# Kernel tuning notes

Measured on AMD Instinct MI355X. Metric: run time of the kernel, lower is better.

Reference implementation:

```python
import jax, jax.numpy as jnp
import numpy as np

IMG = 640
STRIDES = (8, 16, 32)
A = 5            # anchors per level
NC = 80          # num classes
IOU_TH = 0.5
NEG_RATIO = 1.0


def make_priors():
    scales = [1.0, 1.5, 2.0, 2.5, 3.0]
    out = []
    for s in STRIDES:
        f = IMG // s
        ys, xs = np.meshgrid(np.arange(f), np.arange(f), indexing='ij')
        cx = ((xs + 0.5) / f).ravel()
        cy = ((ys + 0.5) / f).ravel()
        for sc in scales:  # anchor-major to match merge_features (A, h, w) order
            wh = min(sc * 4.0 * s / IMG, 1.0)
            out.append(np.stack([cx, cy, np.full_like(cx, wh), np.full_like(cx, wh)], 1))
    return np.concatenate(out, 0).astype(np.float32)  # [42000, 4] cxcywh


def merge_features(feats):
    outs = []
    for feat in feats:
        n, c, h, w = feat.shape
        f = feat.reshape(n, A, c // A, h, w).transpose(0, 1, 3, 4, 2)
        outs.append(f.reshape(n, A * h * w, c // A))
    return jnp.concatenate(outs, axis=1)  # [n, M, 85]


def box_iou_cxcywh(a, b):
    # a [T,4], b [M,4] (cx,cy,w,h) -> IoU [T,M]
    a1 = jnp.concatenate([a[:, :2] - a[:, 2:] / 2, a[:, :2] + a[:, 2:] / 2], -1)
    b1 = jnp.concatenate([b[:, :2] - b[:, 2:] / 2, b[:, :2] + b[:, 2:] / 2], -1)
    tl = jnp.maximum(a1[:, None, :2], b1[None, :, :2])
    br = jnp.minimum(a1[:, None, 2:], b1[None, :, 2:])
    wh = jnp.clip(br - tl, 0.0)
    inter = wh[..., 0] * wh[..., 1]
    area_a = a[:, 2] * a[:, 3]
    area_b = b[:, 2] * b[:, 3]
    return inter / (area_a[:, None] + area_b[None, :] - inter + 1e-9)


def build_targets(targets, priors, batch):
    ious = box_iou_cxcywh(targets[:, 2:6], priors)  # [Nt, M]
    Nt, M = ious.shape
    img_ids = targets[:, 0].astype(jnp.int32)

    def per_image(i):
        valid = img_ids == i  # [Nt]
        iv = jnp.where(valid[:, None], ious, -1.0)
        best_gt_overlap = iv.max(0)            # [M]
        best_gt_idx = iv.argmax(0)             # [M]
        best_prior_idx = iv.argmax(1)          # [Nt]
        # torch: index_fill_(1) then sequential best_gt_overlap[best_prior_idx[j]] = j
        local_j = (jnp.cumsum(valid.astype(jnp.int32)) - 1).astype(jnp.float32)
        scat_idx = jnp.where(valid, best_prior_idx, M)  # drop invalid rows
        best_gt_overlap = best_gt_overlap.at[scat_idx].set(local_j, mode='drop')
        bbox = targets[best_gt_idx, 2:6]
        clss = targets[best_gt_idx, 1] + 1.0
        clss = jnp.where(best_gt_overlap < IOU_TH, 0.0, clss)
        t_xy = (bbox[:, :2] - priors[:, :2]) / priors[:, 2:]
        t_wh = jnp.log(bbox[:, 2:] / priors[:, 2:])
        return t_xy, t_wh, clss

    return jax.vmap(per_image)(jnp.arange(batch))  # [B,M,2],[B,M,2],[B,M]


def _smooth_l1(x):
    ax = jnp.abs(x)
    return jnp.where(ax < 1.0, 0.5 * ax * ax, ax - 0.5)


def compute_loss(preds, priors, targets):
    n, m, _ = preds.shape
    t_xy, t_wh, t_cls = build_targets(targets, priors, n)
    pos = t_cls > 0
    posf = pos.astype(preds.dtype)
    num_pos = posf.sum()

    # lbox: smooth L1 on xy and wh over positives (mean over pos*2 elements each)
    den2 = jnp.maximum(num_pos * 2.0, 1.0)
    lbox = (_smooth_l1(preds[..., 0:2] - t_xy) * posf[..., None]).sum() / den2 \
         + (_smooth_l1(preds[..., 2:4] - t_wh) * posf[..., None]).sum() / den2

    # lcls: cross entropy over positives, labels = t_cls - 1
    labels = jnp.clip(t_cls.astype(jnp.int32) - 1, 0, NC - 1)
    logz = jax.nn.log_softmax(preds[..., 5:], axis=-1)
    ce = -jnp.take_along_axis(logz, labels[..., None], axis=-1)[..., 0]
    lcls = (ce * posf).sum() / jnp.maximum(num_pos, 1.0)

    # hard negative mining (no grad): double argsort rank trick
    obj = preds[..., 4]
    loss_c = jax.lax.stop_gradient(-jax.nn.log_sigmoid(obj))
    loss_c = jnp.where(pos, 0.0, loss_c)
    order = jnp.argsort(-loss_c, axis=-1)
    rank = jnp.argsort(order, axis=-1)
    num_neg = jnp.minimum(NEG_RATIO * num_pos, m - num_pos)
    neg = rank.astype(preds.dtype) < num_neg
    sel = (pos | neg).astype(preds.dtype)

    # lobj: BCE-with-logits over pos|neg
    z = posf
    bce = jnp.maximum(obj, 0.0) - obj * z + jnp.log1p(jnp.exp(-jnp.abs(obj)))
    lobj = (bce * sel).sum() / jnp.maximum(sel.sum(), 1.0)

    loss = lbox + lcls + lobj
    return jnp.stack([loss, lbox, lobj, lcls])


def setup_inputs() -> dict:
    key = jax.random.key(0)
    ks = jax.random.split(key, 6)
    feat0 = jax.random.normal(ks[0], (8, 425, 80, 80), jnp.float32)
    feat1 = jax.random.normal(ks[1], (8, 425, 40, 40), jnp.float32)
    feat2 = jax.random.normal(ks[2], (8, 425, 20, 20), jnp.float32)
    B, T = 8, 20
    img = jnp.repeat(jnp.arange(B, dtype=jnp.float32), T)
    cls = jax.random.randint(ks[3], (B * T,), 0, NC).astype(jnp.float32)
    cxcy = jax.random.uniform(ks[4], (B * T, 2), minval=0.2, maxval=0.8)
    wh = jax.random.uniform(ks[5], (B * T, 2), minval=0.05, maxval=0.3)
    targets = jnp.concatenate([img[:, None], cls[:, None], cxcy, wh], 1)
    priors = jnp.asarray(make_priors())
    return {"feat0": feat0, "feat1": feat1, "feat2": feat2,
            "targets": targets, "priors": priors}


def reference(feat0, feat1, feat2, targets, priors):
    preds = merge_features([feat0, feat1, feat2])  # [8, 42000, 85]
    return compute_loss(preds, priors, targets)    # [loss, lbox, lobj, lcls]
```

## Files before the change

kernel.cpp:

```cpp
#include <hip/hip_runtime.h>
#include <math.h>

#define MTOT 42000
#define NB 8
#define NCLS 80
#define CAP_LIST 4096
#define MAXT 256
#define NT_MAX 2048
#define GX_MAIN 165
#define NBLK_MAIN (GX_MAIN*NB)
#define NCH 32
#define CS 1313

#define O_OVR 0
#define O_GIX (O_OVR + NB*MTOT*4)
#define O_LSC (O_GIX + NB*MTOT*4)
#define O_BCE (O_LSC + NB*MTOT*4)
#define O_BPI (O_BCE + NB*MTOT*4)
#define O_LJ  (O_BPI + NT_MAX*4)
#define O_LST (O_LJ + NT_MAX*4)
#define O_BPP (O_LST + NB*MAXT*4)
#define O_PA  (O_BPP + NT_MAX*NCH*8)
#define O_PN  (O_PA + NBLK_MAIN*16)
#define O_P2  (O_PN + NBLK_MAIN*4)
#define O_BINL (O_P2 + NBLK_MAIN*8)
#define O_CNT (O_BINL + NB*CAP_LIST*2*4)
#define O_HA  (((O_CNT + NB*4 + 255)/256)*256)
#define O_HB  (O_HA + NB*256*4)
#define O_ACC (O_HB + NB*256*4)
#define O_ACCI (O_ACC + 64)
#define O_ZEND (O_ACCI + 256)
#define ZWORDS ((O_ZEND - O_HA)/4)
#define ZBLK ((ZWORDS + 255)/256)

__device__ __forceinline__ float iou_cxcywh(float acx,float acy,float aw,float ah,
                                            float bcx,float bcy,float bw,float bh){
  float ax0=acx-aw*0.5f, ay0=acy-ah*0.5f, ax1=acx+aw*0.5f, ay1=acy+ah*0.5f;
  float bx0=bcx-bw*0.5f, by0=bcy-bh*0.5f, bx1=bcx+bw*0.5f, by1=bcy+bh*0.5f;
  float tlx=fmaxf(ax0,bx0), tly=fmaxf(ay0,by0);
  float brx=fminf(ax1,bx1), bry=fminf(ay1,by1);
  float wx=fmaxf(brx-tlx,0.f), wy=fmaxf(bry-tly,0.f);
  float inter=wx*wy;
  return inter/(aw*ah+bw*bh-inter+1e-9f);
}

__device__ __forceinline__ float sl1(float x){
  float ax=fabsf(x); return ax<1.f ? 0.5f*ax*ax : ax-0.5f;
}

__device__ __forceinline__ void feat_base(const float* f0,const float* f1,const float* f2,
                                          int i,int m,const float** basep,int* hwp){
  const float* fp; int hw, loc;
  if(m<32000){ fp=f0; hw=6400; loc=m; }
  else if(m<40000){ fp=f1; hw=1600; loc=m-32000; }
  else { fp=f2; hw=400; loc=m-40000; }
  int a=loc/hw, p=loc-a*hw;
  *basep = fp + (size_t)(i*425 + a*85)*(size_t)hw + p;
  *hwp = hw;
}

__global__ void k_init(const float* __restrict__ tg, int nt, int* __restrict__ list,
                       int* __restrict__ cnt, int* __restrict__ lj,
                       unsigned* __restrict__ zbase){
  int bx=blockIdx.x, tid=threadIdx.x;
  if(bx<ZBLK){
    int w=bx*256+tid;
    if(w<ZWORDS) zbase[w]=0u;
    return;
  }
  if(bx==ZBLK && tid<NB){
    int c=0;
    for(int q=0;q<nt;q++) if((int)tg[q*6]==tid) c++;
    cnt[tid]=c;
  }
  int t=(bx-ZBLK)*256+tid;
  if(t>=nt) return;
  int img=(int)tg[t*6];
  int j=0;
  for(int q=0;q<t;q++) if((int)tg[q*6]==img) j++;
  lj[t]=j;
  if(img>=0 && img<NB && j<MAXT) list[img*MAXT+j]=t;
}

__global__ void k_match(const float* __restrict__ tg, const float* __restrict__ priors,
                        const int* __restrict__ list, const int* __restrict__ cnt,
                        float* __restrict__ ovr, int* __restrict__ gix){
  __shared__ float st[MAXT*6];
  __shared__ int   sidx[MAXT];
  int i = blockIdx.y;
  int n = min(cnt[i],MAXT);
  for(int j=threadIdx.x;j<n;j+=blockDim.x){
    int t=list[i*MAXT+j];
    sidx[j]=t;
    #pragma unroll
    for(int q=0;q<6;q++) st[j*6+q]=tg[t*6+q];
  }
  __syncthreads();
  int m = blockIdx.x*blockDim.x + threadIdx.x;
  if(m>=MTOT) return;
  float4 pr = ((const float4*)priors)[m];
  float maxv=-1.0f; int bi=0;
  for(int j=0;j<n;j++){
    float v=iou_cxcywh(st[j*6+2],st[j*6+3],st[j*6+4],st[j*6+5], pr.x,pr.y,pr.z,pr.w);
    if(v>maxv){ maxv=v; bi=sidx[j]; }
  }
  ovr[i*MTOT+m]=maxv; gix[i*MTOT+m]=bi;
}

__global__ void k_bpA(const float* __restrict__ tg, const float* __restrict__ priors,
                      int nt, unsigned long long* __restrict__ part){
  __shared__ unsigned long long s[256];
  int t=blockIdx.y; if(t>=nt) return;
  int c=blockIdx.x;
  float acx=tg[t*6+2],acy=tg[t*6+3],aw=tg[t*6+4],ah=tg[t*6+5];
  int m0=c*CS, m1=min(m0+CS,MTOT);
  float bv=-1.f; int bm=0;
  for(int m=m0+threadIdx.x;m<m1;m+=blockDim.x){
    float4 pr=((const float4*)priors)[m];
    float v=iou_cxcywh(acx,acy,aw,ah,pr.x,pr.y,pr.z,pr.w);
    if(v>bv){ bv=v; bm=m; }
  }
  unsigned long long p = (bv<0.f) ? 0ull
      : (((unsigned long long)__float_as_uint(bv))<<32) | (unsigned)(~bm);
  s[threadIdx.x]=p;
  __syncthreads();
  for(int o=128;o>0;o>>=1){
    if(threadIdx.x<o){ if(s[threadIdx.x+o]>s[threadIdx.x]) s[threadIdx.x]=s[threadIdx.x+o]; }
    __syncthreads();
  }
  if(threadIdx.x==0) part[(size_t)t*NCH+c]=s[0];
}

__global__ void k_bpB(const unsigned long long* __restrict__ part, int nt,
                      int* __restrict__ bpi){
  __shared__ unsigned long long s[64];
  int t=blockIdx.x; if(t>=nt) return;
  int l=threadIdx.x;
  s[l]=(l<NCH)? part[(size_t)t*NCH+l] : 0ull;
  __syncthreads();
  for(int o=32;o>0;o>>=1){
    if(l<o){ if(s[l+o]>s[l]) s[l]=s[l+o]; }
    __syncthreads();
  }
  if(l==0) bpi[t]=~((unsigned)(s[0]&0xFFFFFFFFull));
}

__global__ void k_scatter(const float* __restrict__ tg, int nt,
                          const int* __restrict__ bpi, const int* __restrict__ lj,
                          float* __restrict__ ovr){
  int t=blockIdx.x*blockDim.x+threadIdx.x;
  if(t>=nt) return;
  int img=(int)tg[t*6];
  if(img<0||img>=NB) return;
  int myp=bpi[t];
  for(int q=t+1;q<nt;q++)
    if((int)tg[q*6]==img && bpi[q]==myp) return;
  ovr[img*MTOT+myp]=(float)lj[t];
}

__global__ void k_main(const float* __restrict__ f0,const float* __restrict__ f1,const float* __restrict__ f2,
                       const float* __restrict__ tg,const float* __restrict__ priors,
                       const float* __restrict__ ovr,const int* __restrict__ gix,
                       float* __restrict__ lsc,float* __restrict__ bcearr,
                       unsigned* __restrict__ histA,
                       float4* __restrict__ partA,int* __restrict__ partN){
  __shared__ unsigned h[256];
  __shared__ float sxy[4],swh[4],sbp[4],sce[4];
  __shared__ int snp[4];
  int tid=threadIdx.x;
  h[tid]=0;
  __syncthreads();
  int i=blockIdx.y;
  int m=blockIdx.x*blockDim.x+tid;
  int lane=tid&63, wid=tid>>6;
  bool valid=(m<MTOT);

  float lxy=0.f,lwh=0.f,bcep=0.f; int npos=0; bool pos=false; int gi=0;
  if(valid){
    int gid=i*MTOT+m;
    const float* base; int hw;
    feat_base(f0,f1,f2,i,m,&base,&hw);
    float ov=ovr[gid]; gi=gix[gid];
    float tc=tg[gi*6+1]+1.0f;
    pos=(ov>=0.5f)&&(tc>0.f);
    float obj=base[(size_t)4*hw];
    float sp=log1pf(expf(-fabsf(obj)));
    float bce=fmaxf(obj,0.f)-(pos?obj:0.f)+sp;
    float lc=pos?0.f:(fmaxf(-obj,0.f)+sp);
    lsc[gid]=lc; bcearr[gid]=bce;
    atomicAdd(&h[__float_as_uint(lc)>>24],1u);
    if(pos){
      npos=1; bcep=bce;
      float4 pr=((const float4*)priors)[m];
      float bx=tg[gi*6+2],by=tg[gi*6+3],bw=tg[gi*6+4],bh=tg[gi*6+5];
      float tx=(bx-pr.x)/pr.z, ty=(by-pr.y)/pr.w;
      float tw=logf(bw/pr.z), th=logf(bh/pr.w);
      lxy=sl1(base[0]-tx)+sl1(base[(size_t)hw]-ty);
      lwh=sl1(base[(size_t)2*hw]-tw)+sl1(base[(size_t)3*hw]-th);
    }
  }

  float wce=0.f;
  unsigned long long mask=__ballot(valid&&pos);
  while(mask){
    int s=__ffsll(mask)-1;
    mask&=mask-1;
    int m_s=__shfl(m,s);
    int gi_s=__shfl(gi,s);
    const float* bs; int hws;
    feat_base(f0,f1,f2,i,m_s,&bs,&hws);
    int label=(int)(tg[gi_s*6+1]+1.0f)-1;
    label=min(NCLS-1,max(0,label));
    float v0=bs[(size_t)(5+lane)*hws];
    float v1=(lane<16)?bs[(size_t)(69+lane)*hws]:-3.0e38f;
    float mx=fmaxf(v0,v1);
    #pragma unroll
    for(int o=32;o>0;o>>=1) mx=fmaxf(mx,__shfl_xor(mx,o));
    float se=expf(v0-mx)+((lane<16)?expf(v1-mx):0.f);
    float xl=((lane==label)?v0:0.f)+((lane<16&&lane+64==label)?v1:0.f);
    #pragma unroll
    for(int o=32;o>0;o>>=1){ se+=__shfl_xor(se,o); xl+=__shfl_xor(xl,o); }
    wce+=logf(se)+mx-xl;
  }

  #pragma unroll
  for(int o=32;o>0;o>>=1){
    lxy+=__shfl_xor(lxy,o); lwh+=__shfl_xor(lwh,o);
    bcep+=__shfl_xor(bcep,o); npos+=__shfl_xor(npos,o);
  }
  if(lane==0){ sxy[wid]=lxy; swh[wid]=lwh; sbp[wid]=bcep; sce[wid]=wce; snp[wid]=npos; }
  __syncthreads();
  unsigned c=h[tid];
  if(c) atomicAdd(&histA[i*256+tid],c);
  if(tid==0){
    float4 pa;
    pa.x=sxy[0]+sxy[1]+sxy[2]+sxy[3];
    pa.y=swh[0]+swh[1]+swh[2]+swh[3];
    pa.z=sce[0]+sce[1]+sce[2]+sce[3];
    pa.w=sbp[0]+sbp[1]+sbp[2]+sbp[3];
    int bid=blockIdx.y*gridDim.x+blockIdx.x;
    partA[bid]=pa;
    partN[bid]=snp[0]+snp[1]+snp[2]+snp[3];
  }
}

__global__ void k_redscanA(const float4* __restrict__ partA,const int* __restrict__ partN,
                           const unsigned* __restrict__ histA,
                           float* __restrict__ accf,int* __restrict__ acci){
  __shared__ int an[256];
  __shared__ float a0[256],a1[256],a2[256],a3[256];
  __shared__ unsigned a[256];
  int t=threadIdx.x, i=blockIdx.x;
  bool lead=(i==0);
  int n=0; float x=0,y=0,z=0,w=0;
  for(int b=t;b<NBLK_MAIN;b+=256){
    n+=partN[b];
    if(lead){ float4 p=partA[b]; x+=p.x; y+=p.y; z+=p.z; w+=p.w; }
  }
  an[t]=n;
  if(lead){ a0[t]=x; a1[t]=y; a2[t]=z; a3[t]=w; }
  __syncthreads();
  for(int o=128;o>0;o>>=1){
    if(t<o){
      an[t]+=an[t+o];
      if(lead){ a0[t]+=a0[t+o]; a1[t]+=a1[t+o]; a2[t]+=a2[t+o]; a3[t]+=a3[t+o]; }
    }
    __syncthreads();
  }
  int np=an[0];
  if(lead && t==0){ accf[0]=a0[0]; accf[1]=a1[0]; accf[2]=a2[0]; accf[3]=a3[0]; acci[0]=np; }
  a[t]=histA[i*256+t];
  __syncthreads();
  if(t==0){
    int k=min(np, MTOT-np);
    if(k<=0){ acci[2+i]=0x7fffffff; acci[10+i]=0; return; }
    int run=0;
    for(int c=255;c>=0;c--){
      int cb=(int)a[c];
      if(run<k && run+cb>=k){ acci[2+i]=c; acci[10+i]=k-run; return; }
      run+=cb;
    }
    acci[2+i]=0; acci[10+i]=k-run;
  }
}

__global__ void k_histB(const float* __restrict__ lsc, const int* __restrict__ acci,
                        unsigned* __restrict__ histB){
  __shared__ unsigned h[256];
  h[threadIdx.x]=0;
  __syncthreads();
  int i=blockIdx.y;
  int ca=acci[2+i];
  int m=blockIdx.x*blockDim.x+threadIdx.x;
  if(m<MTOT && ca!=0x7fffffff){
    unsigned u=__float_as_uint(lsc[i*MTOT+m]);
    if((int)(u>>24)==ca) atomicAdd(&h[(u>>16)&0xFF],1u);
  }
  __syncthreads();
  unsigned c=h[threadIdx.x];
  if(c) atomicAdd(&histB[i*256+threadIdx.x],c);
}

__device__ __forceinline__ void fine_scan(const unsigned* hb,int ca,int kres,int* bs_out,int* r_out){
  if(ca==0x7fffffff){ *bs_out=0x7fffffff; *r_out=0; return; }
  int run=0, bs=-1, r=0;
  for(int f=255;f>=0;f--){
    int cb=(int)hb[f];
    if(run<kres && run+cb>=kres){ bs=(ca<<8)|f; r=kres-run; break; }
    run+=cb;
  }
  if(bs<0){ bs=(ca<<8); r=kres-run; }
  *bs_out=bs; *r_out=r;
}

__global__ void k_select(const float* __restrict__ lsc,const float* __restrict__ bcearr,
                         const unsigned* __restrict__ histB,
                         int* __restrict__ acci,float2* __restrict__ part2,
                         int* __restrict__ binlist){
  __shared__ unsigned hb[256];
  __shared__ int sbs;
  __shared__ float ss[4]; __shared__ float sc[4];
  int tid=threadIdx.x, lane=tid&63, wid=tid>>6;
  int i=blockIdx.y;
  int ca=acci[2+i], kres=acci[10+i];
  hb[tid]=(ca==0x7fffffff)?0u:histB[i*256+tid];
  __syncthreads();
  if(tid==0){ int bs,r; fine_scan(hb,ca,kres,&bs,&r); sbs=bs; }
  __syncthreads();
  int bs_=sbs;
  int m=blockIdx.x*blockDim.x+tid;
  float s=0.f, c=0.f;
  if(m<MTOT){
    int gid=i*MTOT+m;
    unsigned u=__float_as_uint(lsc[gid]);
    int bin=(int)(u>>16);
    if(bin>bs_){ s=bcearr[gid]; c=1.f; }
    else if(bin==bs_){
      int idx=atomicAdd(&acci[18+i],1);
      if(idx<CAP_LIST){
        binlist[((size_t)i*CAP_LIST+idx)*2  ]=(int)u;
        binlist[((size_t)i*CAP_LIST+idx)*2+1]=gid;
      }
    }
  }
  #pragma unroll
  for(int o=32;o>0;o>>=1){ s+=__shfl_xor(s,o); c+=__shfl_xor(c,o); }
  if(lane==0){ ss[wid]=s; sc[wid]=c; }
  __syncthreads();
  if(tid==0) part2[blockIdx.y*gridDim.x+blockIdx.x]=make_float2(ss[0]+ss[1]+ss[2]+ss[3], sc[0]+sc[1]+sc[2]+sc[3]);
}

__global__ void k_ties(const float* __restrict__ bcearr,int* __restrict__ acci,
                       float* __restrict__ accf,const int* __restrict__ binlist,
                       const unsigned* __restrict__ histB){
  __shared__ unsigned hb[256];
  __shared__ int sbs, sr;
  int i=blockIdx.x, tid=threadIdx.x;
  int ca=acci[2+i], kres=acci[10+i];
  hb[tid]=(ca==0x7fffffff)?0u:histB[i*256+tid];
  __syncthreads();
  if(tid==0){ int bs,r; fine_scan(hb,ca,kres,&bs,&r); sbs=bs; sr=r; }
  __syncthreads();
  if(sbs==0x7fffffff) return;
  int n=min(acci[18+i],CAP_LIST);
  int r=sr;
  for(int e=tid;e<n;e+=blockDim.x){
    unsigned ue=(unsigned)binlist[((size_t)i*CAP_LIST+e)*2];
    int ge=binlist[((size_t)i*CAP_LIST+e)*2+1];
    int rank=0;
    for(int q=0;q<n;q++){
      unsigned uq=(unsigned)binlist[((size_t)i*CAP_LIST+q)*2];
      int gq=binlist[((size_t)i*CAP_LIST+q)*2+1];
      rank += ((uq>ue) || (uq==ue && gq<ge)) ? 1 : 0;
    }
    if(rank<r){
      atomicAdd(&accf[5], bcearr[ge]);
      atomicAdd(&acci[1], 1);
    }
  }
}

__global__ void k_final(const float* __restrict__ accf,const int* __restrict__ acci,
                        const float2* __restrict__ part2,float* __restrict__ out){
  __shared__ float ssum[256]; __shared__ float scnt[256];
  int t=threadIdx.x;
  float s=0.f,c=0.f;
  for(int b=t;b<NBLK_MAIN;b+=256){ float2 p=part2[b]; s+=p.x; c+=p.y; }
  ssum[t]=s; scnt[t]=c;
  __syncthreads();
  for(int o=128;o>0;o>>=1){
    if(t<o){ ssum[t]+=ssum[t+o]; scnt[t]+=scnt[t+o]; }
    __syncthreads();
  }
  if(t==0){
    int np=acci[0];
    float npf=(float)np;
    float den2=fmaxf(2.f*npf,1.f);
    float lbox=accf[0]/den2 + accf[1]/den2;
    float lcls=accf[2]/fmaxf(npf,1.f);
    float negsum=ssum[0]+accf[5];
    float negcnt=scnt[0]+(float)acci[1];
    float selc=npf+negcnt;
    float lobj=(accf[3]+negsum)/fmaxf(selc,1.f);
    out[0]=lbox+lcls+lobj;
    out[1]=lbox;
    out[2]=lobj;
    out[3]=lcls;
  }
}

extern "C" void kernel_launch(void* const* d_in, const int* in_sizes, int n_in,
                              void* d_out, int out_size, void* d_ws, size_t ws_size,
                              hipStream_t stream) {
  const float* f0=(const float*)d_in[0];
  const float* f1=(const float*)d_in[1];
  const float* f2=(const float*)d_in[2];
  const float* tg=(const float*)d_in[3];
  const float* priors=(const float*)d_in[4];
  int nt = in_sizes[3]/6;
  if(nt>NT_MAX) nt=NT_MAX;

  char* ws=(char*)d_ws;
  float*    ovr    =(float*)   (ws+O_OVR);
  int*      gix    =(int*)     (ws+O_GIX);
  float*    lsc    =(float*)   (ws+O_LSC);
  float*    bcearr =(float*)   (ws+O_BCE);
  int*      bpi    =(int*)     (ws+O_BPI);
  int*      lj     =(int*)     (ws+O_LJ);
  int*      list   =(int*)     (ws+O_LST);
  unsigned long long* bpp=(unsigned long long*)(ws+O_BPP);
  float4*   partA  =(float4*)  (ws+O_PA);
  int*      partN  =(int*)     (ws+O_PN);
  float2*   part2  =(float2*)  (ws+O_P2);
  int*      binlist=(int*)     (ws+O_BINL);
  int*      cnt    =(int*)     (ws+O_CNT);
  unsigned* histA  =(unsigned*)(ws+O_HA);
  unsigned* histB  =(unsigned*)(ws+O_HB);
  float*    accf   =(float*)   (ws+O_ACC);
  int*      acci   =(int*)     (ws+O_ACCI);
  unsigned* zbase  =(unsigned*)(ws+O_HA);

  int ntb=(nt+255)/256;
  k_init<<<ZBLK+ntb,256,0,stream>>>(tg,nt,list,cnt,lj,zbase);
  dim3 gm(GX_MAIN, NB);
  k_match<<<gm,256,0,stream>>>(tg,priors,list,cnt,ovr,gix);
  dim3 gbp(NCH, nt);
  k_bpA<<<gbp,256,0,stream>>>(tg,priors,nt,bpp);
  k_bpB<<<nt,64,0,stream>>>(bpp,nt,bpi);
  k_scatter<<<ntb,256,0,stream>>>(tg,nt,bpi,lj,ovr);
  k_main<<<gm,256,0,stream>>>(f0,f1,f2,tg,priors,ovr,gix,lsc,bcearr,histA,partA,partN);
  k_redscanA<<<NB,256,0,stream>>>(partA,partN,histA,accf,acci);
  k_histB<<<gm,256,0,stream>>>(lsc,acci,histB);
  k_select<<<gm,256,0,stream>>>(lsc,bcearr,histB,acci,part2,binlist);
  k_ties<<<NB,256,0,stream>>>(bcearr,acci,accf,binlist,histB);
  k_final<<<1,256,0,stream>>>(accf,acci,part2,(float*)d_out);
}
```

Measured before the change: 151.5 us.

## Merge independent stages into heterogeneous launches and cut kernel count

Several independent stages now share one launch with a per-block role: prior matching, objectness gathering and per-target best-prior search go into one grid, and the negative histogram pass runs alongside the positive box/class loss. The best-prior reduction and scatter collapse into one single-block kernel, and the tie resolution merges with the final reduction. The aim is to cut launch overhead and serialization across about eleven small kernels. In exchange it adds an extra objectness buffer round trip and serializes tie work into one block.

Result: slower. 247.2 us (+63.2%).

```diff
diff --git a/kernel.cpp b/kernel.cpp
--- a/kernel.cpp
+++ b/kernel.cpp
@@ -14,22 +14,21 @@
 
 #define O_OVR 0
 #define O_GIX (O_OVR + NB*MTOT*4)
-#define O_LSC (O_GIX + NB*MTOT*4)
+#define O_OBJ (O_GIX + NB*MTOT*4)
+#define O_LSC (O_OBJ + NB*MTOT*4)
 #define O_BCE (O_LSC + NB*MTOT*4)
-#define O_BPI (O_BCE + NB*MTOT*4)
-#define O_LJ  (O_BPI + NT_MAX*4)
-#define O_LST (O_LJ + NT_MAX*4)
-#define O_BPP (O_LST + NB*MAXT*4)
+#define O_LST (O_BCE + NB*MTOT*4)
+#define O_LJ  (O_LST + NB*MAXT*4)
+#define O_CNT (O_LJ + NT_MAX*4)
+#define O_BPP (((O_CNT + 64 + 7)/8)*8)
 #define O_PA  (O_BPP + NT_MAX*NCH*8)
 #define O_PN  (O_PA + NBLK_MAIN*16)
 #define O_P2  (O_PN + NBLK_MAIN*4)
 #define O_BINL (O_P2 + NBLK_MAIN*8)
-#define O_CNT (O_BINL + NB*CAP_LIST*2*4)
-#define O_HA  (((O_CNT + NB*4 + 255)/256)*256)
+#define O_HA  (((O_BINL + NB*CAP_LIST*2*4 + 255)/256)*256)
 #define O_HB  (O_HA + NB*256*4)
-#define O_ACC (O_HB + NB*256*4)
-#define O_ACCI (O_ACC + 64)
-#define O_ZEND (O_ACCI + 256)
+#define O_ACCI (O_HB + NB*256*4)
+#define O_ZEND (O_ACCI + 128)
 #define ZWORDS ((O_ZEND - O_HA)/4)
 #define ZBLK ((ZWORDS + 255)/256)
 
@@ -59,6 +58,18 @@
   *hwp = hw;
 }
 
+__device__ __forceinline__ void fine_scan(const unsigned* hb,int ca,int kres,int* bs_out,int* r_out){
+  if(ca==0x7fffffff){ *bs_out=0x7fffffff; *r_out=0; return; }
+  int run=0, bs=-1, r=0;
+  for(int f=255;f>=0;f--){
+    int cb=(int)hb[f];
+    if(run<kres && run+cb>=kres){ bs=(ca<<8)|f; r=kres-run; break; }
+    run+=cb;
+  }
+  if(bs<0){ bs=(ca<<8); r=kres-run; }
+  *bs_out=bs; *r_out=r;
+}
+
 __global__ void k_init(const float* __restrict__ tg, int nt, int* __restrict__ list,
                        int* __restrict__ cnt, int* __restrict__ lj,
                        unsigned* __restrict__ zbase){
@@ -82,235 +93,233 @@
   if(img>=0 && img<NB && j<MAXT) list[img*MAXT+j]=t;
 }
 
-__global__ void k_match(const float* __restrict__ tg, const float* __restrict__ priors,
-                        const int* __restrict__ list, const int* __restrict__ cnt,
-                        float* __restrict__ ovr, int* __restrict__ gix){
+__global__ void k_big1(const float* __restrict__ f0,const float* __restrict__ f1,const float* __restrict__ f2,
+                       const float* __restrict__ tg,const float* __restrict__ priors,
+                       const int* __restrict__ list,const int* __restrict__ cnt,int nt,
+                       float* __restrict__ ovr,int* __restrict__ gix,
+                       float* __restrict__ objc,unsigned long long* __restrict__ bpp){
   __shared__ float st[MAXT*6];
-  __shared__ int   sidx[MAXT];
-  int i = blockIdx.y;
-  int n = min(cnt[i],MAXT);
-  for(int j=threadIdx.x;j<n;j+=blockDim.x){
-    int t=list[i*MAXT+j];
-    sidx[j]=t;
-    #pragma unroll
-    for(int q=0;q<6;q++) st[j*6+q]=tg[t*6+q];
-  }
-  __syncthreads();
-  int m = blockIdx.x*blockDim.x + threadIdx.x;
-  if(m>=MTOT) return;
-  float4 pr = ((const float4*)priors)[m];
-  float maxv=-1.0f; int bi=0;
-  for(int j=0;j<n;j++){
-    float v=iou_cxcywh(st[j*6+2],st[j*6+3],st[j*6+4],st[j*6+5], pr.x,pr.y,pr.z,pr.w);
-    if(v>maxv){ maxv=v; bi=sidx[j]; }
-  }
-  ovr[i*MTOT+m]=maxv; gix[i*MTOT+m]=bi;
-}
-
-__global__ void k_bpA(const float* __restrict__ tg, const float* __restrict__ priors,
-                      int nt, unsigned long long* __restrict__ part){
-  __shared__ unsigned long long s[256];
-  int t=blockIdx.y; if(t>=nt) return;
-  int c=blockIdx.x;
-  float acx=tg[t*6+2],acy=tg[t*6+3],aw=tg[t*6+4],ah=tg[t*6+5];
-  int m0=c*CS, m1=min(m0+CS,MTOT);
-  float bv=-1.f; int bm=0;
-  for(int m=m0+threadIdx.x;m<m1;m+=blockDim.x){
+  __shared__ int sidx[MAXT];
+  __shared__ unsigned long long su[256];
+  int b=blockIdx.x, tid=threadIdx.x;
+  if(b<NBLK_MAIN){
+    int i=b/GX_MAIN, cb=b-(b/GX_MAIN)*GX_MAIN;
+    int n=min(cnt[i],MAXT);
+    for(int j=tid;j<n;j+=256){
+      int t=list[i*MAXT+j];
+      sidx[j]=t;
+      #pragma unroll
+      for(int q=0;q<6;q++) st[j*6+q]=tg[t*6+q];
+    }
+    __syncthreads();
+    int m=cb*256+tid;
+    if(m>=MTOT) return;
     float4 pr=((const float4*)priors)[m];
-    float v=iou_cxcywh(acx,acy,aw,ah,pr.x,pr.y,pr.z,pr.w);
-    if(v>bv){ bv=v; bm=m; }
-  }
-  unsigned long long p = (bv<0.f) ? 0ull
-      : (((unsigned long long)__float_as_uint(bv))<<32) | (unsigned)(~bm);
-  s[threadIdx.x]=p;
-  __syncthreads();
-  for(int o=128;o>0;o>>=1){
-    if(threadIdx.x<o){ if(s[threadIdx.x+o]>s[threadIdx.x]) s[threadIdx.x]=s[threadIdx.x+o]; }
-    __syncthreads();
-  }
-  if(threadIdx.x==0) part[(size_t)t*NCH+c]=s[0];
-}
-
-__global__ void k_bpB(const unsigned long long* __restrict__ part, int nt,
-                      int* __restrict__ bpi){
-  __shared__ unsigned long long s[64];
-  int t=blockIdx.x; if(t>=nt) return;
-  int l=threadIdx.x;
-  s[l]=(l<NCH)? part[(size_t)t*NCH+l] : 0ull;
-  __syncthreads();
-  for(int o=32;o>0;o>>=1){
-    if(l<o){ if(s[l+o]>s[l]) s[l]=s[l+o]; }
-    __syncthreads();
-  }
-  if(l==0) bpi[t]=~((unsigned)(s[0]&0xFFFFFFFFull));
-}
-
-__global__ void k_scatter(const float* __restrict__ tg, int nt,
-                          const int* __restrict__ bpi, const int* __restrict__ lj,
-                          float* __restrict__ ovr){
-  int t=blockIdx.x*blockDim.x+threadIdx.x;
-  if(t>=nt) return;
-  int img=(int)tg[t*6];
-  if(img<0||img>=NB) return;
-  int myp=bpi[t];
-  for(int q=t+1;q<nt;q++)
-    if((int)tg[q*6]==img && bpi[q]==myp) return;
-  ovr[img*MTOT+myp]=(float)lj[t];
-}
-
-__global__ void k_main(const float* __restrict__ f0,const float* __restrict__ f1,const float* __restrict__ f2,
-                       const float* __restrict__ tg,const float* __restrict__ priors,
-                       const float* __restrict__ ovr,const int* __restrict__ gix,
-                       float* __restrict__ lsc,float* __restrict__ bcearr,
-                       unsigned* __restrict__ histA,
-                       float4* __restrict__ partA,int* __restrict__ partN){
-  __shared__ unsigned h[256];
-  __shared__ float sxy[4],swh[4],sbp[4],sce[4];
-  __shared__ int snp[4];
-  int tid=threadIdx.x;
-  h[tid]=0;
-  __syncthreads();
-  int i=blockIdx.y;
-  int m=blockIdx.x*blockDim.x+tid;
-  int lane=tid&63, wid=tid>>6;
-  bool valid=(m<MTOT);
-
-  float lxy=0.f,lwh=0.f,bcep=0.f; int npos=0; bool pos=false; int gi=0;
-  if(valid){
-    int gid=i*MTOT+m;
+    float maxv=-1.f; int bi=0;
+    for(int j=0;j<n;j++){
+      float v=iou_cxcywh(st[j*6+2],st[j*6+3],st[j*6+4],st[j*6+5],pr.x,pr.y,pr.z,pr.w);
+      if(v>maxv){ maxv=v; bi=sidx[j]; }
+    }
+    ovr[i*MTOT+m]=maxv; gix[i*MTOT+m]=bi;
+  } else if(b<2*NBLK_MAIN){
+    int idx=b-NBLK_MAIN;
+    int i=idx/GX_MAIN, cb=idx-(idx/GX_MAIN)*GX_MAIN;
+    int m=cb*256+tid;
+    if(m>=MTOT) return;
     const float* base; int hw;
     feat_base(f0,f1,f2,i,m,&base,&hw);
-    float ov=ovr[gid]; gi=gix[gid];
-    float tc=tg[gi*6+1]+1.0f;
-    pos=(ov>=0.5f)&&(tc>0.f);
-    float obj=base[(size_t)4*hw];
+    objc[i*MTOT+m]=base[(size_t)4*hw];
+  } else {
+    int idx=b-2*NBLK_MAIN;
+    int t=idx/NCH, c=idx-(idx/NCH)*NCH;
+    float acx=tg[t*6+2],acy=tg[t*6+3],aw=tg[t*6+4],ah=tg[t*6+5];
+    int m0=c*CS, m1=min(m0+CS,MTOT);
+    float bv=-1.f; int bm=0;
+    for(int m=m0+tid;m<m1;m+=256){
+      float4 pr=((const float4*)priors)[m];
+      float v=iou_cxcywh(acx,acy,aw,ah,pr.x,pr.y,pr.z,pr.w);
+      if(v>bv){ bv=v; bm=m; }
+    }
+    unsigned long long p=(bv<0.f)?0ull
+        :(((unsigned long long)__float_as_uint(bv))<<32)|(unsigned)(~bm);
+    su[tid]=p;
+    __syncthreads();
+    for(int o=128;o>0;o>>=1){
+      if(tid<o){ if(su[tid+o]>su[tid]) su[tid]=su[tid+o]; }
+      __syncthreads();
+    }
+    if(tid==0) bpp[(size_t)t*NCH+c]=su[0];
+  }
+}
+
+__global__ void k_bpsc(const float* __restrict__ tg,int nt,
+                       const unsigned long long* __restrict__ bpp,
+                       const int* __restrict__ lj,float* __restrict__ ovr){
+  __shared__ int tbp[NT_MAX];
+  __shared__ int timg[NT_MAX];
+  int tid=threadIdx.x;
+  for(int t=tid;t<nt;t+=256){
+    unsigned long long best=0ull;
+    const unsigned long long* pp=&bpp[(size_t)t*NCH];
+    for(int c=0;c<NCH;c++){ unsigned long long v=pp[c]; if(v>best) best=v; }
+    int bm=~((unsigned)(best&0xFFFFFFFFull));
+    tbp[t]=min(max(bm,0),MTOT-1);
+    timg[t]=(int)tg[t*6];
+  }
+  __syncthreads();
+  for(int t=tid;t<nt;t+=256){
+    int img=timg[t];
+    if(img<0||img>=NB) continue;
+    int myp=tbp[t];
+    bool last=true;
+    for(int q=t+1;q<nt;q++) if(timg[q]==img&&tbp[q]==myp){ last=false; break; }
+    if(last) ovr[img*MTOT+myp]=(float)lj[t];
+  }
+}
+
+__global__ void k_lc(const float* __restrict__ tg,const float* __restrict__ objc,
+                     const float* __restrict__ ovr,const int* __restrict__ gix,int nt,
+                     float* __restrict__ lsc,float* __restrict__ bcearr,
+                     unsigned* __restrict__ histA,int* __restrict__ partN){
+  __shared__ unsigned h[256];
+  __shared__ int snp[4];
+  int tid=threadIdx.x, lane=tid&63, wid=tid>>6;
+  h[tid]=0u;
+  __syncthreads();
+  int i=blockIdx.y;
+  int m=blockIdx.x*256+tid;
+  int npos=0;
+  if(m<MTOT){
+    int gid=i*MTOT+m;
+    float ov=ovr[gid];
+    int gi=min(max(gix[gid],0),nt-1);
+    float tc=tg[gi*6+1]+1.f;
+    bool pos=(ov>=0.5f)&&(tc>0.f);
+    float obj=objc[gid];
     float sp=log1pf(expf(-fabsf(obj)));
     float bce=fmaxf(obj,0.f)-(pos?obj:0.f)+sp;
     float lc=pos?0.f:(fmaxf(-obj,0.f)+sp);
     lsc[gid]=lc; bcearr[gid]=bce;
     atomicAdd(&h[__float_as_uint(lc)>>24],1u);
-    if(pos){
-      npos=1; bcep=bce;
-      float4 pr=((const float4*)priors)[m];
-      float bx=tg[gi*6+2],by=tg[gi*6+3],bw=tg[gi*6+4],bh=tg[gi*6+5];
-      float tx=(bx-pr.x)/pr.z, ty=(by-pr.y)/pr.w;
-      float tw=logf(bw/pr.z), th=logf(bh/pr.w);
-      lxy=sl1(base[0]-tx)+sl1(base[(size_t)hw]-ty);
-      lwh=sl1(base[(size_t)2*hw]-tw)+sl1(base[(size_t)3*hw]-th);
-    }
-  }
-
-  float wce=0.f;
-  unsigned long long mask=__ballot(valid&&pos);
-  while(mask){
-    int s=__ffsll(mask)-1;
-    mask&=mask-1;
-    int m_s=__shfl(m,s);
-    int gi_s=__shfl(gi,s);
-    const float* bs; int hws;
-    feat_base(f0,f1,f2,i,m_s,&bs,&hws);
-    int label=(int)(tg[gi_s*6+1]+1.0f)-1;
-    label=min(NCLS-1,max(0,label));
-    float v0=bs[(size_t)(5+lane)*hws];
-    float v1=(lane<16)?bs[(size_t)(69+lane)*hws]:-3.0e38f;
-    float mx=fmaxf(v0,v1);
+    npos=pos?1:0;
+  }
+  #pragma unroll
+  for(int o=32;o>0;o>>=1) npos+=__shfl_xor(npos,o);
+  if(lane==0) snp[wid]=npos;
+  __syncthreads();
+  unsigned hc=h[tid];
+  if(hc) atomicAdd(&histA[i*256+tid],hc);
+  if(tid==0) partN[blockIdx.y*GX_MAIN+blockIdx.x]=snp[0]+snp[1]+snp[2]+snp[3];
+}
+
+__global__ void k_redscanA(const int* __restrict__ partN,const unsigned* __restrict__ histA,
+                           int* __restrict__ acci){
+  __shared__ int an[256];
+  __shared__ unsigned h[256];
+  int t=threadIdx.x, b=blockIdx.x;
+  int n=0;
+  for(int e=t;e<NBLK_MAIN;e+=256) n+=partN[e];
+  an[t]=n;
+  __syncthreads();
+  for(int o=128;o>0;o>>=1){ if(t<o) an[t]+=an[t+o]; __syncthreads(); }
+  int np=an[0];
+  if(b==0&&t==0) acci[0]=np;
+  h[t]=histA[b*256+t];
+  __syncthreads();
+  if(t==0){
+    int kk=min(np,MTOT-np);
+    if(kk<=0){ acci[2+b]=0x7fffffff; acci[10+b]=0; }
+    else{
+      int run=0, ca=-1, kres=0;
+      for(int c2=255;c2>=0;c2--){
+        int cbn=(int)h[c2];
+        if(run<kk&&run+cbn>=kk){ ca=c2; kres=kk-run; break; }
+        run+=cbn;
+      }
+      if(ca<0){ ca=0; kres=kk-run; }
+      acci[2+b]=ca; acci[10+b]=kres;
+    }
+  }
+}
+
+__global__ void k_big2(const float* __restrict__ f0,const float* __restrict__ f1,const float* __restrict__ f2,
+                       const float* __restrict__ tg,const float* __restrict__ priors,
+                       const float* __restrict__ ovr,const int* __restrict__ gix,
+                       const float* __restrict__ lsc,const float* __restrict__ bcearr,
+                       const int* __restrict__ acci,int nt,
+                       unsigned* __restrict__ histB,float4* __restrict__ partA){
+  __shared__ unsigned h[256];
+  __shared__ float rA[4],rB[4],rC[4],rD[4];
+  int b=blockIdx.x, tid=threadIdx.x, lane=tid&63, wid=tid>>6;
+  if(b<NBLK_MAIN){
+    h[tid]=0u;
+    __syncthreads();
+    int i=b/GX_MAIN, cb=b-(b/GX_MAIN)*GX_MAIN;
+    int ca=acci[2+i];
+    int m=cb*256+tid;
+    if(m<MTOT && ca!=0x7fffffff){
+      unsigned u=__float_as_uint(lsc[i*MTOT+m]);
+      if((int)(u>>24)==ca) atomicAdd(&h[(u>>16)&0xFF],1u);
+    }
+    __syncthreads();
+    unsigned c=h[tid];
+    if(c) atomicAdd(&histB[i*256+tid],c);
+  } else {
+    int idx=b-NBLK_MAIN;
+    int i=idx/GX_MAIN, cb=idx-(idx/GX_MAIN)*GX_MAIN;
+    int m=cb*256+tid;
+    bool valid=(m<MTOT);
+    float lxy=0.f,lwh=0.f,bcep=0.f,wce=0.f;
+    bool pos=false; int gi=0;
+    if(valid){
+      int gid=i*MTOT+m;
+      float ov=ovr[gid];
+      gi=min(max(gix[gid],0),nt-1);
+      float tc=tg[gi*6+1]+1.f;
+      pos=(ov>=0.5f)&&(tc>0.f);
+      if(pos){
+        const float* base; int hw;
+        feat_base(f0,f1,f2,i,m,&base,&hw);
+        bcep=bcearr[gid];
+        float4 pr=((const float4*)priors)[m];
+        float bx=tg[gi*6+2],by=tg[gi*6+3],bw=tg[gi*6+4],bh=tg[gi*6+5];
+        float tx=(bx-pr.x)/pr.z, ty=(by-pr.y)/pr.w;
+        float tw=logf(bw/pr.z), th=logf(bh/pr.w);
+        lxy=sl1(base[0]-tx)+sl1(base[(size_t)hw]-ty);
+        lwh=sl1(base[(size_t)2*hw]-tw)+sl1(base[(size_t)3*hw]-th);
+      }
+    }
+    unsigned long long mask=__ballot(valid&&pos);
+    while(mask){
+      int s=__ffsll(mask)-1;
+      mask&=mask-1;
+      int m_s=__shfl(m,s);
+      int gi_s=__shfl(gi,s);
+      const float* bs2; int hws;
+      feat_base(f0,f1,f2,i,m_s,&bs2,&hws);
+      int label=(int)(tg[gi_s*6+1]+1.f)-1;
+      label=min(NCLS-1,max(0,label));
+      float v0=bs2[(size_t)(5+lane)*hws];
+      float v1=(lane<16)?bs2[(size_t)(69+lane)*hws]:-3.0e38f;
+      float mx=fmaxf(v0,v1);
+      #pragma unroll
+      for(int o=32;o>0;o>>=1) mx=fmaxf(mx,__shfl_xor(mx,o));
+      float se=expf(v0-mx)+((lane<16)?expf(v1-mx):0.f);
+      float xl=((lane==label)?v0:0.f)+((lane<16&&lane+64==label)?v1:0.f);
+      #pragma unroll
+      for(int o=32;o>0;o>>=1){ se+=__shfl_xor(se,o); xl+=__shfl_xor(xl,o); }
+      wce+=logf(se)+mx-xl;
+    }
     #pragma unroll
-    for(int o=32;o>0;o>>=1) mx=fmaxf(mx,__shfl_xor(mx,o));
-    float se=expf(v0-mx)+((lane<16)?expf(v1-mx):0.f);
-    float xl=((lane==label)?v0:0.f)+((lane<16&&lane+64==label)?v1:0.f);
-    #pragma unroll
-    for(int o=32;o>0;o>>=1){ se+=__shfl_xor(se,o); xl+=__shfl_xor(xl,o); }
-    wce+=logf(se)+mx-xl;
-  }
-
-  #pragma unroll
-  for(int o=32;o>0;o>>=1){
-    lxy+=__shfl_xor(lxy,o); lwh+=__shfl_xor(lwh,o);
-    bcep+=__shfl_xor(bcep,o); npos+=__shfl_xor(npos,o);
-  }
-  if(lane==0){ sxy[wid]=lxy; swh[wid]=lwh; sbp[wid]=bcep; sce[wid]=wce; snp[wid]=npos; }
-  __syncthreads();
-  unsigned c=h[tid];
-  if(c) atomicAdd(&histA[i*256+tid],c);
-  if(tid==0){
-    float4 pa;
-    pa.x=sxy[0]+sxy[1]+sxy[2]+sxy[3];
-    pa.y=swh[0]+swh[1]+swh[2]+swh[3];
-    pa.z=sce[0]+sce[1]+sce[2]+sce[3];
-    pa.w=sbp[0]+sbp[1]+sbp[2]+sbp[3];
-    int bid=blockIdx.y*gridDim.x+blockIdx.x;
-    partA[bid]=pa;
-    partN[bid]=snp[0]+snp[1]+snp[2]+snp[3];
-  }
-}
-
-__global__ void k_redscanA(const float4* __restrict__ partA,const int* __restrict__ partN,
-                           const unsigned* __restrict__ histA,
-                           float* __restrict__ accf,int* __restrict__ acci){
-  __shared__ int an[256];
-  __shared__ float a0[256],a1[256],a2[256],a3[256];
-  __shared__ unsigned a[256];
-  int t=threadIdx.x, i=blockIdx.x;
-  bool lead=(i==0);
-  int n=0; float x=0,y=0,z=0,w=0;
-  for(int b=t;b<NBLK_MAIN;b+=256){
-    n+=partN[b];
-    if(lead){ float4 p=partA[b]; x+=p.x; y+=p.y; z+=p.z; w+=p.w; }
-  }
-  an[t]=n;
-  if(lead){ a0[t]=x; a1[t]=y; a2[t]=z; a3[t]=w; }
-  __syncthreads();
-  for(int o=128;o>0;o>>=1){
-    if(t<o){
-      an[t]+=an[t+o];
-      if(lead){ a0[t]+=a0[t+o]; a1[t]+=a1[t+o]; a2[t]+=a2[t+o]; a3[t]+=a3[t+o]; }
-    }
-    __syncthreads();
-  }
-  int np=an[0];
-  if(lead && t==0){ accf[0]=a0[0]; accf[1]=a1[0]; accf[2]=a2[0]; accf[3]=a3[0]; acci[0]=np; }
-  a[t]=histA[i*256+t];
-  __syncthreads();
-  if(t==0){
-    int k=min(np, MTOT-np);
-    if(k<=0){ acci[2+i]=0x7fffffff; acci[10+i]=0; return; }
-    int run=0;
-    for(int c=255;c>=0;c--){
-      int cb=(int)a[c];
-      if(run<k && run+cb>=k){ acci[2+i]=c; acci[10+i]=k-run; return; }
-      run+=cb;
-    }
-    acci[2+i]=0; acci[10+i]=k-run;
-  }
-}
-
-__global__ void k_histB(const float* __restrict__ lsc, const int* __restrict__ acci,
-                        unsigned* __restrict__ histB){
-  __shared__ unsigned h[256];
-  h[threadIdx.x]=0;
-  __syncthreads();
-  int i=blockIdx.y;
-  int ca=acci[2+i];
-  int m=blockIdx.x*blockDim.x+threadIdx.x;
-  if(m<MTOT && ca!=0x7fffffff){
-    unsigned u=__float_as_uint(lsc[i*MTOT+m]);
-    if((int)(u>>24)==ca) atomicAdd(&h[(u>>16)&0xFF],1u);
-  }
-  __syncthreads();
-  unsigned c=h[threadIdx.x];
-  if(c) atomicAdd(&histB[i*256+threadIdx.x],c);
-}
-
-__device__ __forceinline__ void fine_scan(const unsigned* hb,int ca,int kres,int* bs_out,int* r_out){
-  if(ca==0x7fffffff){ *bs_out=0x7fffffff; *r_out=0; return; }
-  int run=0, bs=-1, r=0;
-  for(int f=255;f>=0;f--){
-    int cb=(int)hb[f];
-    if(run<kres && run+cb>=kres){ bs=(ca<<8)|f; r=kres-run; break; }
-    run+=cb;
-  }
-  if(bs<0){ bs=(ca<<8); r=kres-run; }
-  *bs_out=bs; *r_out=r;
+    for(int o=32;o>0;o>>=1){
+      lxy+=__shfl_xor(lxy,o); lwh+=__shfl_xor(lwh,o); bcep+=__shfl_xor(bcep,o);
+    }
+    if(lane==0){ rA[wid]=lxy; rB[wid]=lwh; rC[wid]=wce; rD[wid]=bcep; }
+    __syncthreads();
+    if(tid==0)
+      partA[idx]=make_float4(rA[0]+rA[1]+rA[2]+rA[3], rB[0]+rB[1]+rB[2]+rB[3],
+                             rC[0]+rC[1]+rC[2]+rC[3], rD[0]+rD[1]+rD[2]+rD[3]);
+  }
 }
 
 __global__ void k_select(const float* __restrict__ lsc,const float* __restrict__ bcearr,
@@ -328,7 +337,7 @@
   if(tid==0){ int bs,r; fine_scan(hb,ca,kres,&bs,&r); sbs=bs; }
   __syncthreads();
   int bs_=sbs;
-  int m=blockIdx.x*blockDim.x+tid;
+  int m=blockIdx.x*256+tid;
   float s=0.f, c=0.f;
   if(m<MTOT){
     int gid=i*MTOT+m;
@@ -350,58 +359,69 @@
   if(tid==0) part2[blockIdx.y*gridDim.x+blockIdx.x]=make_float2(ss[0]+ss[1]+ss[2]+ss[3], sc[0]+sc[1]+sc[2]+sc[3]);
 }
 
-__global__ void k_ties(const float* __restrict__ bcearr,int* __restrict__ acci,
-                       float* __restrict__ accf,const int* __restrict__ binlist,
-                       const unsigned* __restrict__ histB){
+__global__ void k_tf(const float4* __restrict__ partA,const float2* __restrict__ part2,
+                     const float* __restrict__ bcearr,const unsigned* __restrict__ histB,
+                     const int* __restrict__ acci,const int* __restrict__ binlist,
+                     float* __restrict__ out){
+  __shared__ float a0[256],a1[256],a2[256],a3[256],s0[256],s1[256];
   __shared__ unsigned hb[256];
   __shared__ int sbs, sr;
-  int i=blockIdx.x, tid=threadIdx.x;
-  int ca=acci[2+i], kres=acci[10+i];
-  hb[tid]=(ca==0x7fffffff)?0u:histB[i*256+tid];
-  __syncthreads();
-  if(tid==0){ int bs,r; fine_scan(hb,ca,kres,&bs,&r); sbs=bs; sr=r; }
-  __syncthreads();
-  if(sbs==0x7fffffff) return;
-  int n=min(acci[18+i],CAP_LIST);
-  int r=sr;
-  for(int e=tid;e<n;e+=blockDim.x){
-    unsigned ue=(unsigned)binlist[((size_t)i*CAP_LIST+e)*2];
-    int ge=binlist[((size_t)i*CAP_LIST+e)*2+1];
-    int rank=0;
-    for(int q=0;q<n;q++){
-      unsigned uq=(unsigned)binlist[((size_t)i*CAP_LIST+q)*2];
-      int gq=binlist[((size_t)i*CAP_LIST+q)*2+1];
-      rank += ((uq>ue) || (uq==ue && gq<ge)) ? 1 : 0;
-    }
-    if(rank<r){
-      atomicAdd(&accf[5], bcearr[ge]);
-      atomicAdd(&acci[1], 1);
-    }
-  }
-}
-
-__global__ void k_final(const float* __restrict__ accf,const int* __restrict__ acci,
-                        const float2* __restrict__ part2,float* __restrict__ out){
-  __shared__ float ssum[256]; __shared__ float scnt[256];
-  int t=threadIdx.x;
-  float s=0.f,c=0.f;
-  for(int b=t;b<NBLK_MAIN;b+=256){ float2 p=part2[b]; s+=p.x; c+=p.y; }
-  ssum[t]=s; scnt[t]=c;
+  int tid=threadIdx.x, lane=tid&63, wid=tid>>6;
+  float x=0,y=0,z=0,w=0,ns=0,nc=0;
+  for(int e=tid;e<NBLK_MAIN;e+=256){
+    float4 p=partA[e]; x+=p.x; y+=p.y; z+=p.z; w+=p.w;
+    float2 q=part2[e]; ns+=q.x; nc+=q.y;
+  }
+  a0[tid]=x; a1[tid]=y; a2[tid]=z; a3[tid]=w; s0[tid]=ns; s1[tid]=nc;
   __syncthreads();
   for(int o=128;o>0;o>>=1){
-    if(t<o){ ssum[t]+=ssum[t+o]; scnt[t]+=scnt[t+o]; }
-    __syncthreads();
-  }
-  if(t==0){
+    if(tid<o){
+      a0[tid]+=a0[tid+o]; a1[tid]+=a1[tid+o]; a2[tid]+=a2[tid+o]; a3[tid]+=a3[tid+o];
+      s0[tid]+=s0[tid+o]; s1[tid]+=s1[tid+o];
+    }
+    __syncthreads();
+  }
+  float sum_xy=a0[0], sum_wh=a1[0], sum_ce=a2[0], sum_bcep=a3[0];
+  float negsum=s0[0], negcnt=s1[0];
+  float tsum=0.f; int tcnt=0;
+  for(int i=0;i<NB;i++){
+    int ca=acci[2+i], kres=acci[10+i];
+    __syncthreads();
+    hb[tid]=(ca==0x7fffffff)?0u:histB[i*256+tid];
+    __syncthreads();
+    if(tid==0){ int bs,r; fine_scan(hb,ca,kres,&bs,&r); sbs=bs; sr=r; }
+    __syncthreads();
+    if(sbs==0x7fffffff) continue;
+    int n=min(acci[18+i],CAP_LIST);
+    int r=sr;
+    for(int e=tid;e<n;e+=256){
+      unsigned ue=(unsigned)binlist[((size_t)i*CAP_LIST+e)*2];
+      int ge=binlist[((size_t)i*CAP_LIST+e)*2+1];
+      int rank=0;
+      for(int q=0;q<n;q++){
+        unsigned uq=(unsigned)binlist[((size_t)i*CAP_LIST+q)*2];
+        int gq=binlist[((size_t)i*CAP_LIST+q)*2+1];
+        rank += ((uq>ue)||(uq==ue&&gq<ge))?1:0;
+      }
+      if(rank<r){ tsum+=bcearr[ge]; tcnt++; }
+    }
+  }
+  float ftc=(float)tcnt;
+  #pragma unroll
+  for(int o=32;o>0;o>>=1){ tsum+=__shfl_xor(tsum,o); ftc+=__shfl_xor(ftc,o); }
+  __syncthreads();
+  if(lane==0){ a0[wid]=tsum; a1[wid]=ftc; }
+  __syncthreads();
+  if(tid==0){
+    negsum+=a0[0]+a0[1]+a0[2]+a0[3];
+    negcnt+=a1[0]+a1[1]+a1[2]+a1[3];
     int np=acci[0];
     float npf=(float)np;
     float den2=fmaxf(2.f*npf,1.f);
-    float lbox=accf[0]/den2 + accf[1]/den2;
-    float lcls=accf[2]/fmaxf(npf,1.f);
-    float negsum=ssum[0]+accf[5];
-    float negcnt=scnt[0]+(float)acci[1];
+    float lbox=sum_xy/den2+sum_wh/den2;
+    float lcls=sum_ce/fmaxf(npf,1.f);
     float selc=npf+negcnt;
-    float lobj=(accf[3]+negsum)/fmaxf(selc,1.f);
+    float lobj=(sum_bcep+negsum)/fmaxf(selc,1.f);
     out[0]=lbox+lcls+lobj;
     out[1]=lbox;
     out[2]=lobj;
@@ -419,39 +439,35 @@
   const float* priors=(const float*)d_in[4];
   int nt = in_sizes[3]/6;
   if(nt>NT_MAX) nt=NT_MAX;
+  if(nt<1) nt=1;
 
   char* ws=(char*)d_ws;
   float*    ovr    =(float*)   (ws+O_OVR);
   int*      gix    =(int*)     (ws+O_GIX);
+  float*    objc   =(float*)   (ws+O_OBJ);
   float*    lsc    =(float*)   (ws+O_LSC);
   float*    bcearr =(float*)   (ws+O_BCE);
-  int*      bpi    =(int*)     (ws+O_BPI);
+  int*      list   =(int*)     (ws+O_LST);
   int*      lj     =(int*)     (ws+O_LJ);
-  int*      list   =(int*)     (ws+O_LST);
+  int*      cnt    =(int*)     (ws+O_CNT);
   unsigned long long* bpp=(unsigned long long*)(ws+O_BPP);
   float4*   partA  =(float4*)  (ws+O_PA);
   int*      partN  =(int*)     (ws+O_PN);
   float2*   part2  =(float2*)  (ws+O_P2);
   int*      binlist=(int*)     (ws+O_BINL);
-  int*      cnt    =(int*)     (ws+O_CNT);
   unsigned* histA  =(unsigned*)(ws+O_HA);
   unsigned* histB  =(unsigned*)(ws+O_HB);
-  float*    accf   =(float*)   (ws+O_ACC);
   int*      acci   =(int*)     (ws+O_ACCI);
   unsigned* zbase  =(unsigned*)(ws+O_HA);
 
   int ntb=(nt+255)/256;
   k_init<<<ZBLK+ntb,256,0,stream>>>(tg,nt,list,cnt,lj,zbase);
+  k_big1<<<2*NBLK_MAIN+nt*NCH,256,0,stream>>>(f0,f1,f2,tg,priors,list,cnt,nt,ovr,gix,objc,bpp);
+  k_bpsc<<<1,256,0,stream>>>(tg,nt,bpp,lj,ovr);
   dim3 gm(GX_MAIN, NB);
-  k_match<<<gm,256,0,stream>>>(tg,priors,list,cnt,ovr,gix);
-  dim3 gbp(NCH, nt);
-  k_bpA<<<gbp,256,0,stream>>>(tg,priors,nt,bpp);
-  k_bpB<<<nt,64,0,stream>>>(bpp,nt,bpi);
-  k_scatter<<<ntb,256,0,stream>>>(tg,nt,bpi,lj,ovr);
-  k_main<<<gm,256,0,stream>>>(f0,f1,f2,tg,priors,ovr,gix,lsc,bcearr,histA,partA,partN);
-  k_redscanA<<<NB,256,0,stream>>>(partA,partN,histA,accf,acci);
-  k_histB<<<gm,256,0,stream>>>(lsc,acci,histB);
+  k_lc<<<gm,256,0,stream>>>(tg,objc,ovr,gix,nt,lsc,bcearr,histA,partN);
+  k_redscanA<<<NB,256,0,stream>>>(partN,histA,acci);
+  k_big2<<<2*NBLK_MAIN,256,0,stream>>>(f0,f1,f2,tg,priors,ovr,gix,lsc,bcearr,acci,nt,histB,partA);
   k_select<<<gm,256,0,stream>>>(lsc,bcearr,histB,acci,part2,binlist);
-  k_ties<<<NB,256,0,stream>>>(bcearr,acci,accf,binlist,histB);
-  k_final<<<1,256,0,stream>>>(accf,acci,part2,(float*)d_out);
-}
+  k_tf<<<1,256,0,stream>>>(partA,part2,bcearr,histB,acci,binlist,(float*)d_out);
+}
```
